# Kernel optimization log

Measured on AMD Instinct MI355X. Metric: run time of the kernel, lower is better.

The kernel has to match this reference:

```python
import jax, jax.numpy as jnp
import numpy as np

N = 100_000          # nodes
E = 800_000          # edges
IN_DIM = 128
OUT_DIM = 128
H = 8                # heads
DK = OUT_DIM // H    # 16
T = 3                # node types
R = 8                # edge relation types
LN_EPS = 1e-5


def setup_inputs():
    key = jax.random.key(0)
    k = jax.random.split(key, 16)
    node_inp = jax.random.normal(k[0], (N, IN_DIM), dtype=jnp.float32)
    node_type = jax.random.randint(k[1], (N,), 0, T)
    edge_index = jax.random.randint(k[2], (2, E), 0, N)
    edge_type = jax.random.randint(k[3], (E,), 0, R)
    edge_sign = jax.random.randint(k[4], (E,), 0, 3) - 1      # values in {-1,0,1}
    edge_distance = jax.random.uniform(k[5], (E,), dtype=jnp.float32) * 2e5
    sc = 1.0 / np.sqrt(IN_DIM)
    Wq = jax.random.normal(k[6], (T, IN_DIM, OUT_DIM), dtype=jnp.float32) * sc
    Wk = jax.random.normal(k[7], (T, IN_DIM, OUT_DIM), dtype=jnp.float32) * sc
    Wv = jax.random.normal(k[8], (T, IN_DIM, OUT_DIM), dtype=jnp.float32) * sc
    bq = jnp.zeros((T, OUT_DIM), jnp.float32)
    bk = jnp.zeros((T, OUT_DIM), jnp.float32)
    bv = jnp.zeros((T, OUT_DIM), jnp.float32)
    rel_q = jax.random.normal(k[9], (R, H, DK), dtype=jnp.float32) * 0.2
    rel_k = jax.random.normal(k[10], (R, H, DK), dtype=jnp.float32) * 0.2
    rel_v = jax.random.normal(k[11], (R, H, DK), dtype=jnp.float32) * 0.2
    rel_bias = jnp.zeros((R, H), jnp.float32)
    ones = jnp.ones((H, DK), dtype=jnp.float32)
    sign_k_fixed = jnp.stack([-ones, ones], axis=0)   # [2,H,DK] buffers (neg,pos)
    sign_v_fixed = jnp.stack([-ones, ones], axis=0)
    sign_k_neutral = jnp.ones((H, DK), jnp.float32)
    sign_v_neutral = jnp.ones((H, DK), jnp.float32)
    dist_alpha = jnp.float32(0.1)
    dist_tau = jnp.float32(1e5)
    skip = jnp.ones((T,), jnp.float32)
    ln_gamma = jnp.ones((T, OUT_DIM), jnp.float32)
    ln_beta = jnp.zeros((T, OUT_DIM), jnp.float32)
    return dict(node_inp=node_inp, node_type=node_type, edge_index=edge_index,
                edge_type=edge_type, edge_sign=edge_sign, edge_distance=edge_distance,
                Wq=Wq, bq=bq, Wk=Wk, bk=bk, Wv=Wv, bv=bv,
                rel_q=rel_q, rel_k=rel_k, rel_v=rel_v, rel_bias=rel_bias,
                sign_k_fixed=sign_k_fixed, sign_v_fixed=sign_v_fixed,
                sign_k_neutral=sign_k_neutral, sign_v_neutral=sign_v_neutral,
                dist_alpha=dist_alpha, dist_tau=dist_tau, skip=skip,
                ln_gamma=ln_gamma, ln_beta=ln_beta)


def reference(node_inp, node_type, edge_index, edge_type, edge_sign, edge_distance,
              Wq, bq, Wk, bk, Wv, bv, rel_q, rel_k, rel_v, rel_bias,
              sign_k_fixed, sign_v_fixed, sign_k_neutral, sign_v_neutral,
              dist_alpha, dist_tau, skip, ln_gamma, ln_beta):
    src, dst = edge_index[0], edge_index[1]
    n = node_inp.shape[0]
    e = src.shape[0]
    # Per-node-type Q/K/V: compute projections for all types [N,T,O], select by type
    # (equivalent to the masked per-type Linear dispatch in the torch code).
    ar = jnp.arange(n)
    Q = (jnp.einsum('nd,tdo->nto', node_inp, Wq) + bq)[ar, node_type].reshape(n, H, DK)
    K = (jnp.einsum('nd,tdo->nto', node_inp, Wk) + bk)[ar, node_type].reshape(n, H, DK)
    V = (jnp.einsum('nd,tdo->nto', node_inp, Wv) + bv)[ar, node_type].reshape(n, H, DK)
    # sign dispatch: -1 -> 0 (neg), +1 -> 1 (pos), anything else -> 2 (neutral)
    sign_idx = jnp.where(edge_sign == -1, 0, jnp.where(edge_sign == 1, 1, 2))
    sign_k_all = jnp.concatenate([sign_k_fixed, sign_k_neutral[None]], axis=0)  # [3,H,DK]
    sign_v_all = jnp.concatenate([sign_v_fixed, sign_v_neutral[None]], axis=0)
    # edge-wise gather + relational modulation
    q_eff = Q[dst] * rel_q[edge_type]                               # [E,H,DK]
    k_eff = K[src] * rel_k[edge_type] * sign_k_all[sign_idx]
    v_eff = V[src] * rel_v[edge_type] * sign_v_all[sign_idx]
    scores = jnp.sum(q_eff * k_eff, axis=-1) / np.sqrt(DK)          # [E,H]
    scores = scores + rel_bias[edge_type]
    phi = dist_alpha * jnp.exp(-edge_distance / (dist_tau + 1e-9))
    scores = scores + phi[:, None]
    # segment softmax over destination nodes
    m = jax.ops.segment_max(scores, dst, num_segments=n)            # [N,H]
    m = jax.lax.stop_gradient(jnp.where(jnp.isfinite(m), m, 0.0))
    es = jnp.exp(scores - m[dst])
    Z = jax.ops.segment_sum(es, dst, num_segments=n)
    attn = es / (Z[dst] + 1e-9)
    # message scatter-aggregate
    msg = (v_eff * attn[:, :, None]).reshape(e, OUT_DIM)
    out = jax.ops.segment_sum(msg, dst, num_segments=n)             # [N,OUT_DIM]
    # per-type gated residual + per-type LayerNorm
    alpha = jax.nn.sigmoid(skip)[node_type][:, None]
    x = alpha * out + (1.0 - alpha) * node_inp
    mu = jnp.mean(x, axis=-1, keepdims=True)
    var = jnp.mean((x - mu) ** 2, axis=-1, keepdims=True)
    xn = (x - mu) * jax.lax.rsqrt(var + LN_EPS)
    return xn * ln_gamma[node_type] + ln_beta[node_type]
```

## Files before the change

kernel.cpp:

```cpp
#include <hip/hip_runtime.h>
#include <hip/hip_bf16.h>

typedef unsigned int uint;
typedef unsigned short ushort;
typedef unsigned long long ull;
typedef __attribute__((ext_vector_type(8))) short short8;
typedef __attribute__((ext_vector_type(4))) float f32x4;

#define WP_ELEMS 147456

__device__ __forceinline__ ushort f2bf(float f) {
  uint x = __float_as_uint(f);
  return (ushort)((x + 0x7fffu + ((x >> 16) & 1u)) >> 16);
}
__device__ __forceinline__ uint packbf(float a, float b) {
  return ((uint)f2bf(b) << 16) | (uint)f2bf(a);
}
__device__ __forceinline__ float bflo(uint u) { return __uint_as_float(u << 16); }
__device__ __forceinline__ float bfhi(uint u) { return __uint_as_float(u & 0xffff0000u); }

__global__ __launch_bounds__(256) void setup_kernel(
    const float* __restrict__ wq, const float* __restrict__ wk, const float* __restrict__ wv,
    const float* __restrict__ rq, const float* __restrict__ rk, const float* __restrict__ rv,
    ushort* __restrict__ Wp, float* __restrict__ ktab, float* __restrict__ vtab,
    const int* __restrict__ ntype, int* __restrict__ cnt,
    const int* __restrict__ edst, int* __restrict__ ecnt, int N, int E) {
  int i = blockIdx.x * 256 + threadIdx.x;
  if (i < WP_ELEMS) {
    int j    = i & 7;
    int lane = (i >> 3) & 63;
    int ot   = (i >> 9) & 7;
    int ks   = (i >> 12) & 3;
    int mt   = i >> 14;
    int mat  = mt / 3;
    int t    = mt - mat * 3;
    int o = ot * 16 + (lane & 15);
    int d = ks * 32 + (lane >> 4) * 8 + j;
    const float* src = (mat == 0) ? wq : (mat == 1) ? wk : wv;
    Wp[i] = f2bf(src[t * 16384 + d * 128 + o]);
  }
  if (i < 1024) {
    ktab[i] = 0.25f * rq[i] * rk[i];
    vtab[i] = rv[i];
  }
  {
    int lane = threadIdx.x & 63;
    int t = (i < N) ? ntype[i] : -1;
#pragma unroll
    for (int tt = 0; tt < 3; ++tt) {
      ull mask = __ballot(t == tt);
      if (mask) {
        int leader = __ffsll((long long)mask) - 1;
        if (lane == leader) atomicAdd(&cnt[tt], __popcll(mask));
      }
    }
  }
  if (i < E) atomicAdd(&ecnt[edst[i]], 1);
}

__global__ void offs_kernel(const int* __restrict__ cnt, int* __restrict__ off) {
  int o = 0;
  off[0] = 0;
  for (int t = 0; t < 3; ++t) {
    o += ((cnt[t] + 63) >> 6) << 6;
    off[t + 1] = o;
  }
}

__global__ __launch_bounds__(256) void fill_kernel(const int* __restrict__ ntype,
                                                   const int* __restrict__ off,
                                                   int* __restrict__ pos,
                                                   int* __restrict__ perm,
                                                   int* __restrict__ pinv, int N) {
  int i = blockIdx.x * 256 + threadIdx.x;
  int lane = threadIdx.x & 63;
  int t = (i < N) ? ntype[i] : -1;
#pragma unroll
  for (int tt = 0; tt < 3; ++tt) {
    ull mask = __ballot(t == tt);
    if (mask) {
      int leader = __ffsll((long long)mask) - 1;
      int base = 0;
      if (lane == leader) base = atomicAdd(&pos[tt], __popcll(mask));
      base = __shfl(base, leader);
      if (t == tt) {
        int rank = __popcll(mask & ((lane == 63) ? 0x7fffffffffffffffull
                                                 : ((1ull << lane) - 1ull)));
        int p = off[tt] + base + rank;
        perm[p] = i;
        pinv[i] = p;
      }
    }
  }
}

__global__ __launch_bounds__(256) void gemm_kernel(
    const float* __restrict__ X, const int* __restrict__ perm,
    const int* __restrict__ off, const ushort* __restrict__ Wp,
    const float* __restrict__ bq, const float* __restrict__ bk, const float* __restrict__ bv,
    float* __restrict__ Qp, uint* __restrict__ KVp) {
  __shared__ __align__(16) char smem[33792];
  __shared__ int prow[64];
  ushort* As = (ushort*)smem;
  float* tbuf = (float*)smem;
  const int tid = threadIdx.x;
  const int base = blockIdx.x * 64;
  const int off1 = off[1], off2 = off[2], off3 = off[3];
  if (base >= off3) return;
  const int t = (base >= off1) + (base >= off2);

  if (tid < 64) prow[tid] = perm[base + tid];
  __syncthreads();
#pragma unroll
  for (int pass = 0; pass < 8; ++pass) {
    int row = pass * 8 + (tid >> 5);
    int dw = tid & 31;
    int p = prow[row];
    uint ux = 0u, uy = 0u;
    if (p >= 0) {
      float4 xv = *(const float4*)(X + (size_t)p * 128 + dw * 4);
      ux = packbf(xv.x, xv.y);
      uy = packbf(xv.z, xv.w);
    }
    uint* s = (uint*)smem + row * 68 + dw * 2;
    s[0] = ux; s[1] = uy;
  }
  __syncthreads();

  const int lane = tid & 63;
  const int w = tid >> 6;
  const int m0 = w * 16;
  const int r = lane & 15;
  const int q = lane >> 4;

  short8 afrag[4];
#pragma unroll
  for (int ks = 0; ks < 4; ++ks)
    afrag[ks] = *(const short8*)(As + (m0 + r) * 136 + ks * 32 + q * 8);
  __syncthreads();

  float* tw = tbuf + w * 2112;
  uint4 ksave[4];
#pragma unroll
  for (int mat = 0; mat < 3; ++mat) {
    f32x4 acc[8];
#pragma unroll
    for (int ot = 0; ot < 8; ++ot) acc[ot] = (f32x4){0.f, 0.f, 0.f, 0.f};

    const ushort* wb = Wp + (size_t)(mat * 3 + t) * 16384 + lane * 8;
#pragma unroll
    for (int ks = 0; ks < 4; ++ks) {
      const ushort* wk_ = wb + ks * 4096;
#pragma unroll
      for (int ot = 0; ot < 8; ++ot) {
        short8 b = *(const short8*)(wk_ + ot * 512);
        acc[ot] = __builtin_amdgcn_mfma_f32_16x16x32_bf16(afrag[ks], b, acc[ot], 0, 0, 0);
      }
    }

    const float* bias = (mat == 0) ? bq : (mat == 1) ? bk : bv;
#pragma unroll
    for (int ot = 0; ot < 8; ++ot) {
      float bi = bias[t * 128 + ot * 16 + r];
#pragma unroll
      for (int reg = 0; reg < 4; ++reg)
        tw[(q * 4 + reg) * 132 + ot * 16 + r] = acc[ot][reg] + bi;
    }
    if (mat == 0) {
#pragma unroll
      for (int p = 0; p < 8; ++p) {
        int f = (p * 64 + lane) * 4;
        int row = f >> 7, col = f & 127;
        float4 val = *(const float4*)(tw + row * 132 + col);
        *(float4*)(Qp + (size_t)(base + m0 + row) * 128 + col) = val;
      }
    } else if (mat == 1) {
#pragma unroll
      for (int p = 0; p < 4; ++p) {
        int g = p * 64 + lane;
        int f = g * 8;
        int row = f >> 7, col = f & 127;
        const float* src = tw + row * 132 + col;
        float4 a4 = *(const float4*)(src);
        float4 b4 = *(const float4*)(src + 4);
        uint4 u;
        u.x = packbf(a4.x, a4.y);
        u.y = packbf(a4.z, a4.w);
        u.z = packbf(b4.x, b4.y);
        u.w = packbf(b4.z, b4.w);
        ksave[p] = u;
      }
    } else {
#pragma unroll
      for (int p = 0; p < 4; ++p) {
        int g = p * 64 + lane;
        int f = g * 8;
        int row = f >> 7, col = f & 127;
        const float* src = tw + row * 132 + col;
        float4 a4 = *(const float4*)(src);
        float4 b4 = *(const float4*)(src + 4);
        uint4 v4;
        v4.x = packbf(a4.x, a4.y);
        v4.y = packbf(a4.z, a4.w);
        v4.z = packbf(b4.x, b4.y);
        v4.w = packbf(b4.z, b4.w);
        uint4 w0, w1;
        w0.x = ksave[p].x; w0.y = v4.x; w0.z = ksave[p].y; w0.w = v4.y;
        w1.x = ksave[p].z; w1.y = v4.z; w1.z = ksave[p].w; w1.w = v4.w;
        uint* dstp = KVp + (size_t)(base + m0 + row) * 128 + col;
        *(uint4*)(dstp) = w0;
        *(uint4*)(dstp + 4) = w1;
      }
    }
  }
}

__global__ __launch_bounds__(256) void csum_kernel(const int* __restrict__ ecnt,
                                                   int* __restrict__ csum, int N) {
  __shared__ int s[4];
  int basei = blockIdx.x * 1024;
  int tid = threadIdx.x;
  int v = 0;
#pragma unroll
  for (int k = 0; k < 4; ++k) {
    int i = basei + k * 256 + tid;
    if (i < N) v += ecnt[i];
  }
#pragma unroll
  for (int m = 1; m < 64; m <<= 1) v += __shfl_xor(v, m);
  if ((tid & 63) == 0) s[tid >> 6] = v;
  __syncthreads();
  if (tid == 0) csum[blockIdx.x] = s[0] + s[1] + s[2] + s[3];
}

__global__ __launch_bounds__(1024) void cscan_kernel(const int* __restrict__ csum,
                                                     int* __restrict__ coff,
                                                     int* __restrict__ rowptrN,
                                                     int NC, int E) {
  __shared__ int sd[32];
  int tid = threadIdx.x, lane = tid & 63, w = tid >> 6;
  int v = (tid < NC) ? csum[tid] : 0;
  int x = v;
#pragma unroll
  for (int d = 1; d < 64; d <<= 1) {
    int t = __shfl_up(x, d);
    if (lane >= d) x += t;
  }
  if (lane == 63) sd[w] = x;
  __syncthreads();
  if (w == 0 && lane < 16) {
    int y = sd[lane];
#pragma unroll
    for (int d = 1; d < 16; d <<= 1) {
      int t = __shfl_up(y, d);
      if (lane >= d) y += t;
    }
    sd[16 + lane] = y;
  }
  __syncthreads();
  int excl = ((w > 0) ? sd[16 + w - 1] : 0) + (x - v);
  if (tid < NC) coff[tid] = excl;
  if (tid == 0) rowptrN[0] = E;
}

__global__ __launch_bounds__(1024) void rowptr_kernel(const int* __restrict__ ecnt,
                                                      const int* __restrict__ coff,
                                                      int* __restrict__ rowptr,
                                                      int* __restrict__ cursor, int N) {
  __shared__ int sd[32];
  int basei = blockIdx.x * 1024;
  int tid = threadIdx.x, lane = tid & 63, w = tid >> 6;
  int i = basei + tid;
  int v = (i < N) ? ecnt[i] : 0;
  int x = v;
#pragma unroll
  for (int d = 1; d < 64; d <<= 1) {
    int t = __shfl_up(x, d);
    if (lane >= d) x += t;
  }
  if (lane == 63) sd[w] = x;
  __syncthreads();
  if (w == 0 && lane < 16) {
    int y = sd[lane];
#pragma unroll
    for (int d = 1; d < 16; d <<= 1) {
      int t = __shfl_up(y, d);
      if (lane >= d) y += t;
    }
    sd[16 + lane] = y;
  }
  __syncthreads();
  int excl = coff[blockIdx.x] + ((w > 0) ? sd[16 + w - 1] : 0) + (x - v);
  if (i < N) { rowptr[i] = excl; cursor[i] = excl; }
}

__global__ __launch_bounds__(256) void scatter_kernel(
    const int* __restrict__ esrc, const int* __restrict__ edst,
    const int* __restrict__ etype, const int* __restrict__ esign,
    const float* __restrict__ edist,
    const float* __restrict__ p_alpha, const float* __restrict__ p_tau,
    const int* __restrict__ pinv, int* __restrict__ cursor,
    int2* __restrict__ erec, int E) {
  int e = blockIdx.x * 256 + threadIdx.x;
  if (e >= E) return;
  int dst = edst[e];
  int p = atomicAdd(&cursor[dst], 1);
  int et = etype[e], sg = esign[e];
  int sbit = (sg == -1) ? 1 : 0;
  float parg = fminf(fmaxf(-edist[e] / (p_tau[0] + 1e-9f), -80.f), 0.f);
  int2 r;
  r.x = pinv[esrc[e]] | (et << 18) | (sbit << 21);
  r.y = __float_as_int(p_alpha[0] * __expf(parg));
  erec[p] = r;
}

struct Pass {
  uint4 kv0, kv1;
  float4 t0, t1;
  float4 v0, v1;
  float bias;
  float sgn;
  int valid;
};

__device__ __forceinline__ Pass fetchp(
    int e0, int row1, const int2* __restrict__ erec,
    const uint* __restrict__ KVp, const float* __restrict__ ktab,
    const float* __restrict__ vtab, const float* __restrict__ rb, int cl) {
  Pass P;
  P.valid = (e0 < row1);
  int e = P.valid ? e0 : (row1 - 1);
  int2 r = erec[e];
  int pk = r.x;
  float phi = __int_as_float(r.y);
  int pe = pk & 0x3ffff;
  int et = (pk >> 18) & 7;
  P.sgn = (pk & (1 << 21)) ? -1.f : 1.f;
  const uint* kvb = KVp + (size_t)pe * 128 + cl * 8;
  P.kv0 = *(const uint4*)(kvb);
  P.kv1 = *(const uint4*)(kvb + 4);
  const float* kb = ktab + et * 128 + cl * 8;
  P.t0 = *(const float4*)(kb);
  P.t1 = *(const float4*)(kb + 4);
  const float* vb = vtab + et * 128 + cl * 8;
  P.v0 = *(const float4*)(vb);
  P.v1 = *(const float4*)(vb + 4);
  P.bias = rb[et * 8 + (cl >> 1)] + phi;
  return P;
}

__device__ __forceinline__ void computep(
    const Pass& P, const float4& q0, const float4& q1, float& z,
    float& a0, float& a1, float& a2, float& a3,
    float& a4, float& a5, float& a6, float& a7) {
  float part = q0.x * (P.t0.x * bflo(P.kv0.x));
  part = fmaf(q0.y, P.t0.y * bfhi(P.kv0.x), part);
  part = fmaf(q0.z, P.t0.z * bflo(P.kv0.z), part);
  part = fmaf(q0.w, P.t0.w * bfhi(P.kv0.z), part);
  part = fmaf(q1.x, P.t1.x * bflo(P.kv1.x), part);
  part = fmaf(q1.y, P.t1.y * bfhi(P.kv1.x), part);
  part = fmaf(q1.z, P.t1.z * bflo(P.kv1.z), part);
  part = fmaf(q1.w, P.t1.w * bfhi(P.kv1.z), part);
  part += __shfl_xor(part, 1);
  float score = fminf(fmaf(P.sgn, part, P.bias), 80.f);
  float es = __expf(score);
  es = P.valid ? es : 0.f;
  z += es;
  float esv = es * P.sgn;
  a0 = fmaf(esv, P.v0.x * bflo(P.kv0.y), a0);
  a1 = fmaf(esv, P.v0.y * bfhi(P.kv0.y), a1);
  a2 = fmaf(esv, P.v0.z * bflo(P.kv0.w), a2);
  a3 = fmaf(esv, P.v0.w * bfhi(P.kv0.w), a3);
  a4 = fmaf(esv, P.v1.x * bflo(P.kv1.y), a4);
  a5 = fmaf(esv, P.v1.y * bfhi(P.kv1.y), a5);
  a6 = fmaf(esv, P.v1.z * bflo(P.kv1.w), a6);
  a7 = fmaf(esv, P.v1.w * bfhi(P.kv1.w), a7);
}

__global__ __launch_bounds__(256) void agg_kernel(
    const float* __restrict__ Qp, const uint* __restrict__ KVp,
    const int* __restrict__ pinv, const int* __restrict__ rowptr,
    const int2* __restrict__ erec,
    const float* __restrict__ rb, const float* __restrict__ ktab,
    const float* __restrict__ vtab,
    const float* __restrict__ X, const int* __restrict__ ntype,
    const float* __restrict__ skip, const float* __restrict__ gamma,
    const float* __restrict__ beta, float* __restrict__ y, int N) {
  const int wslot = blockIdx.x * 4 + (threadIdx.x >> 6);
  const int lane = threadIdx.x & 63;
  const int g = lane >> 4;
  const int cl = lane & 15;
  const int c0 = cl * 8;

  for (int ii = 0; ii < 4; ++ii) {
    int dst = wslot * 4 + ii;
    if (dst >= N) return;

    int pq = pinv[dst];
    int row0 = rowptr[dst], row1 = rowptr[dst + 1];
    const float* qb = Qp + (size_t)pq * 128 + c0;
    float4 q0 = *(const float4*)(qb);
    float4 q1 = *(const float4*)(qb + 4);

    float a0 = 0.f, a1 = 0.f, a2 = 0.f, a3 = 0.f;
    float a4 = 0.f, a5 = 0.f, a6 = 0.f, a7 = 0.f;
    float z = 0.f;

    int deg = row1 - row0;
    if (deg > 0) {
      int np = (deg + 3) >> 2;
      Pass A = fetchp(row0 + g, row1, erec, KVp, ktab, vtab, rb, cl);
      int p = 0;
      while (true) {
        if (p + 1 < np) {
          Pass B = fetchp(row0 + (p + 1) * 4 + g, row1, erec, KVp, ktab, vtab, rb, cl);
          computep(A, q0, q1, z, a0, a1, a2, a3, a4, a5, a6, a7);
          A = B;
          ++p;
        } else {
          computep(A, q0, q1, z, a0, a1, a2, a3, a4, a5, a6, a7);
          break;
        }
      }
    }

#pragma unroll
    for (int m = 16; m < 64; m <<= 1) {
      a0 += __shfl_xor(a0, m); a1 += __shfl_xor(a1, m);
      a2 += __shfl_xor(a2, m); a3 += __shfl_xor(a3, m);
      a4 += __shfl_xor(a4, m); a5 += __shfl_xor(a5, m);
      a6 += __shfl_xor(a6, m); a7 += __shfl_xor(a7, m);
      z  += __shfl_xor(z, m);
    }

    if (lane < 16) {
      float inv = 1.0f / (z + 1e-9f);
      float o0 = a0 * inv, o1 = a1 * inv, o2 = a2 * inv, o3 = a3 * inv;
      float o4 = a4 * inv, o5 = a5 * inv, o6 = a6 * inv, o7 = a7 * inv;

      int t = ntype[dst];
      float a = 1.0f / (1.0f + __expf(-skip[t]));
      float b = 1.0f - a;
      const float* xb = X + (size_t)dst * 128 + c0;
      float4 x0 = *(const float4*)(xb);
      float4 x1 = *(const float4*)(xb + 4);
      float w0 = a * o0 + b * x0.x, w1 = a * o1 + b * x0.y;
      float w2 = a * o2 + b * x0.z, w3 = a * o3 + b * x0.w;
      float w4 = a * o4 + b * x1.x, w5 = a * o5 + b * x1.y;
      float w6 = a * o6 + b * x1.z, w7 = a * o7 + b * x1.w;

      float sum = w0 + w1 + w2 + w3 + w4 + w5 + w6 + w7;
      float sq = w0 * w0 + w1 * w1 + w2 * w2 + w3 * w3 +
                 w4 * w4 + w5 * w5 + w6 * w6 + w7 * w7;
#pragma unroll
      for (int m = 1; m < 16; m <<= 1) {
        sum += __shfl_xor(sum, m);
        sq  += __shfl_xor(sq, m);
      }
      float mean = sum * (1.0f / 128.0f);
      float var = fmaxf(sq * (1.0f / 128.0f) - mean * mean, 0.0f);
      float rstd = rsqrtf(var + 1e-5f);

      const float* gb = gamma + t * 128 + c0;
      const float* bb2 = beta + t * 128 + c0;
      float4 g0 = *(const float4*)(gb);
      float4 g1 = *(const float4*)(gb + 4);
      float4 be0 = *(const float4*)(bb2);
      float4 be1 = *(const float4*)(bb2 + 4);
      float4 r0, r1;
      r0.x = (w0 - mean) * rstd * g0.x + be0.x;
      r0.y = (w1 - mean) * rstd * g0.y + be0.y;
      r0.z = (w2 - mean) * rstd * g0.z + be0.z;
      r0.w = (w3 - mean) * rstd * g0.w + be0.w;
      r1.x = (w4 - mean) * rstd * g1.x + be1.x;
      r1.y = (w5 - mean) * rstd * g1.y + be1.y;
      r1.z = (w6 - mean) * rstd * g1.z + be1.z;
      r1.w = (w7 - mean) * rstd * g1.w + be1.w;
      float* yb = y + (size_t)dst * 128 + c0;
      *(float4*)(yb) = r0;
      *(float4*)(yb + 4) = r1;
    }
  }
}

extern "C" void kernel_launch(void* const* d_in, const int* in_sizes, int n_in,
                              void* d_out, int out_size, void* d_ws, size_t ws_size,
                              hipStream_t stream) {
  const float* X     = (const float*)d_in[0];
  const int*   ntype = (const int*)d_in[1];
  const int*   eidx  = (const int*)d_in[2];
  const int*   etype = (const int*)d_in[3];
  const int*   esign = (const int*)d_in[4];
  const float* edist = (const float*)d_in[5];
  const float* wq = (const float*)d_in[6];
  const float* bq = (const float*)d_in[7];
  const float* wk = (const float*)d_in[8];
  const float* bk = (const float*)d_in[9];
  const float* wv = (const float*)d_in[10];
  const float* bv = (const float*)d_in[11];
  const float* rq = (const float*)d_in[12];
  const float* rk = (const float*)d_in[13];
  const float* rv = (const float*)d_in[14];
  const float* rb = (const float*)d_in[15];

  const int N = in_sizes[1];
  const int E = in_sizes[3];
  const int NP = N + 192;
  const int NC = (N + 1023) / 1024;

  float* ws = (float*)d_ws;
  float* Qp   = ws;
  uint*  KVp  = (uint*)(Qp + (size_t)NP * 128);
  float* ktab = (float*)(KVp + (size_t)NP * 128);
  float* vtab = ktab + 1024;
  ushort* Wp  = (ushort*)(vtab + 1024);
  int* cnt    = (int*)(Wp + WP_ELEMS);
  int* pos    = cnt + 4;
  int* ecnt   = pos + 4;
  int* perm   = ecnt + N;
  int* pinv   = perm + NP;
  int* off    = pinv + N;
  int* rowptr = off + 4;
  int* cursor = rowptr + N + 1;
  int* csum   = cursor + N;
  int* coff   = csum + 1024;
  int2* erec  = (int2*)(coff + 1024);

  hipMemsetAsync(cnt, 0, (size_t)(8 + N) * sizeof(int), stream);
  hipMemsetAsync(perm, 0xFF, (size_t)NP * sizeof(int), stream);

  setup_kernel<<<(E + 255) / 256, 256, 0, stream>>>(
      wq, wk, wv, rq, rk, rv, Wp, ktab, vtab, ntype, cnt, eidx + E, ecnt, N, E);
  offs_kernel<<<1, 1, 0, stream>>>(cnt, off);
  fill_kernel<<<(N + 255) / 256, 256, 0, stream>>>(ntype, off, pos, perm, pinv, N);

  csum_kernel<<<NC, 256, 0, stream>>>(ecnt, csum, N);
  cscan_kernel<<<1, 1024, 0, stream>>>(csum, coff, rowptr + N, NC, E);
  rowptr_kernel<<<NC, 1024, 0, stream>>>(ecnt, coff, rowptr, cursor, N);
  scatter_kernel<<<(E + 255) / 256, 256, 0, stream>>>(
      eidx, eidx + E, etype, esign, edist, (const float*)d_in[20], (const float*)d_in[21],
      pinv, cursor, erec, E);

  gemm_kernel<<<(N + 255) / 64, 256, 0, stream>>>(X, perm, off, Wp, bq, bk, bv, Qp, KVp);

  agg_kernel<<<(N + 15) / 16, 256, 0, stream>>>(Qp, KVp, pinv, rowptr, erec,
                                                rb, ktab, vtab, X, ntype,
                                                (const float*)d_in[22], (const float*)d_in[23],
                                                (const float*)d_in[24], (float*)d_out, N);
}
```

Before: 507.9 us.

## Merge preprocessing kernels and co-launch GEMM with edge scatter

```diff
diff --git a/kernel.cpp b/kernel.cpp
--- a/kernel.cpp
+++ b/kernel.cpp
@@ -58,44 +58,112 @@
   if (i < E) atomicAdd(&ecnt[edst[i]], 1);
 }
 
-__global__ void offs_kernel(const int* __restrict__ cnt, int* __restrict__ off) {
-  int o = 0;
-  off[0] = 0;
-  for (int t = 0; t < 3; ++t) {
-    o += ((cnt[t] + 63) >> 6) << 6;
-    off[t + 1] = o;
-  }
-}
-
-__global__ __launch_bounds__(256) void fill_kernel(const int* __restrict__ ntype,
-                                                   const int* __restrict__ off,
-                                                   int* __restrict__ pos,
-                                                   int* __restrict__ perm,
-                                                   int* __restrict__ pinv, int N) {
-  int i = blockIdx.x * 256 + threadIdx.x;
-  int lane = threadIdx.x & 63;
-  int t = (i < N) ? ntype[i] : -1;
-#pragma unroll
-  for (int tt = 0; tt < 3; ++tt) {
-    ull mask = __ballot(t == tt);
-    if (mask) {
-      int leader = __ffsll((long long)mask) - 1;
-      int base = 0;
-      if (lane == leader) base = atomicAdd(&pos[tt], __popcll(mask));
-      base = __shfl(base, leader);
-      if (t == tt) {
-        int rank = __popcll(mask & ((lane == 63) ? 0x7fffffffffffffffull
-                                                 : ((1ull << lane) - 1ull)));
-        int p = off[tt] + base + rank;
-        perm[p] = i;
-        pinv[i] = p;
-      }
-    }
-  }
-}
-
-__global__ __launch_bounds__(256) void gemm_kernel(
-    const float* __restrict__ X, const int* __restrict__ perm,
+__global__ __launch_bounds__(256) void fc_kernel(
+    const int* __restrict__ ntype, const int* __restrict__ cnt,
+    int* __restrict__ pos, int* __restrict__ perm, int* __restrict__ pinv,
+    int* __restrict__ off,
+    const int* __restrict__ ecnt, int* __restrict__ csum,
+    int N, int fill_blocks) {
+  __shared__ int s[4];
+  int bid = blockIdx.x;
+  if (bid < fill_blocks) {
+    int i = bid * 256 + threadIdx.x;
+    int lane = threadIdx.x & 63;
+    int c0 = cnt[0], c1 = cnt[1];
+    int o1 = ((c0 + 63) >> 6) << 6;
+    int o2 = o1 + (((c1 + 63) >> 6) << 6);
+    if (i == 0) {
+      int c2 = cnt[2];
+      int o3 = o2 + (((c2 + 63) >> 6) << 6);
+      off[0] = 0; off[1] = o1; off[2] = o2; off[3] = o3;
+    }
+    int t = (i < N) ? ntype[i] : -1;
+#pragma unroll
+    for (int tt = 0; tt < 3; ++tt) {
+      ull mask = __ballot(t == tt);
+      if (mask) {
+        int leader = __ffsll((long long)mask) - 1;
+        int base = 0;
+        if (lane == leader) base = atomicAdd(&pos[tt], __popcll(mask));
+        base = __shfl(base, leader);
+        if (t == tt) {
+          int obase = (tt == 0) ? 0 : (tt == 1) ? o1 : o2;
+          int rank = __popcll(mask & ((lane == 63) ? 0x7fffffffffffffffull
+                                                   : ((1ull << lane) - 1ull)));
+          int p = obase + base + rank;
+          perm[p] = i;
+          pinv[i] = p;
+        }
+      }
+    }
+  } else {
+    int cb = bid - fill_blocks;
+    int basei = cb * 1024;
+    int tid = threadIdx.x;
+    int v = 0;
+#pragma unroll
+    for (int k = 0; k < 4; ++k) {
+      int i = basei + k * 256 + tid;
+      if (i < N) v += ecnt[i];
+    }
+#pragma unroll
+    for (int m = 1; m < 64; m <<= 1) v += __shfl_xor(v, m);
+    if ((tid & 63) == 0) s[tid >> 6] = v;
+    __syncthreads();
+    if (tid == 0) csum[cb] = s[0] + s[1] + s[2] + s[3];
+  }
+}
+
+__global__ __launch_bounds__(1024) void rowptr_kernel(const int* __restrict__ ecnt,
+                                                      const int* __restrict__ csum,
+                                                      int* __restrict__ rowptr,
+                                                      int* __restrict__ cursor,
+                                                      int N, int E) {
+  __shared__ int sd[32];
+  __shared__ int sbase;
+  int basei = blockIdx.x * 1024;
+  int tid = threadIdx.x, lane = tid & 63, w = tid >> 6;
+
+  int c = (tid < blockIdx.x) ? csum[tid] : 0;
+#pragma unroll
+  for (int m = 1; m < 64; m <<= 1) c += __shfl_xor(c, m);
+  if (lane == 0) sd[w] = c;
+  __syncthreads();
+  if (tid == 0) {
+    int s = 0;
+#pragma unroll
+    for (int k = 0; k < 16; ++k) s += sd[k];
+    sbase = s;
+    if (blockIdx.x == 0) rowptr[N] = E;
+  }
+  __syncthreads();
+
+  int i = basei + tid;
+  int v = (i < N) ? ecnt[i] : 0;
+  int x = v;
+#pragma unroll
+  for (int d = 1; d < 64; d <<= 1) {
+    int t = __shfl_up(x, d);
+    if (lane >= d) x += t;
+  }
+  if (lane == 63) sd[w] = x;
+  __syncthreads();
+  if (w == 0 && lane < 16) {
+    int y = sd[lane];
+#pragma unroll
+    for (int d = 1; d < 16; d <<= 1) {
+      int t = __shfl_up(y, d);
+      if (lane >= d) y += t;
+    }
+    sd[16 + lane] = y;
+  }
+  __syncthreads();
+  int excl = sbase + ((w > 0) ? sd[16 + w - 1] : 0) + (x - v);
+  if (i < N) { rowptr[i] = excl; cursor[i] = excl; }
+}
+
+__device__ void gemm_body(
+    int bid, const float* __restrict__ X, const int* __restrict__ perm,
     const int* __restrict__ off, const ushort* __restrict__ Wp,
     const float* __restrict__ bq, const float* __restrict__ bk, const float* __restrict__ bv,
     float* __restrict__ Qp, uint* __restrict__ KVp) {
@@ -104,7 +172,7 @@
   ushort* As = (ushort*)smem;
   float* tbuf = (float*)smem;
   const int tid = threadIdx.x;
-  const int base = blockIdx.x * 64;
+  const int base = bid * 64;
   const int off1 = off[1], off2 = off[2], off3 = off[3];
   if (base >= off3) return;
   const int t = (base >= off1) + (base >= off2);
@@ -215,93 +283,23 @@
   }
 }
 
-__global__ __launch_bounds__(256) void csum_kernel(const int* __restrict__ ecnt,
-                                                   int* __restrict__ csum, int N) {
-  __shared__ int s[4];
-  int basei = blockIdx.x * 1024;
-  int tid = threadIdx.x;
-  int v = 0;
-#pragma unroll
-  for (int k = 0; k < 4; ++k) {
-    int i = basei + k * 256 + tid;
-    if (i < N) v += ecnt[i];
-  }
-#pragma unroll
-  for (int m = 1; m < 64; m <<= 1) v += __shfl_xor(v, m);
-  if ((tid & 63) == 0) s[tid >> 6] = v;
-  __syncthreads();
-  if (tid == 0) csum[blockIdx.x] = s[0] + s[1] + s[2] + s[3];
-}
-
-__global__ __launch_bounds__(1024) void cscan_kernel(const int* __restrict__ csum,
-                                                     int* __restrict__ coff,
-                                                     int* __restrict__ rowptrN,
-                                                     int NC, int E) {
-  __shared__ int sd[32];
-  int tid = threadIdx.x, lane = tid & 63, w = tid >> 6;
-  int v = (tid < NC) ? csum[tid] : 0;
-  int x = v;
-#pragma unroll
-  for (int d = 1; d < 64; d <<= 1) {
-    int t = __shfl_up(x, d);
-    if (lane >= d) x += t;
-  }
-  if (lane == 63) sd[w] = x;
-  __syncthreads();
-  if (w == 0 && lane < 16) {
-    int y = sd[lane];
-#pragma unroll
-    for (int d = 1; d < 16; d <<= 1) {
-      int t = __shfl_up(y, d);
-      if (lane >= d) y += t;
-    }
-    sd[16 + lane] = y;
-  }
-  __syncthreads();
-  int excl = ((w > 0) ? sd[16 + w - 1] : 0) + (x - v);
-  if (tid < NC) coff[tid] = excl;
-  if (tid == 0) rowptrN[0] = E;
-}
-
-__global__ __launch_bounds__(1024) void rowptr_kernel(const int* __restrict__ ecnt,
-                                                      const int* __restrict__ coff,
-                                                      int* __restrict__ rowptr,
-                                                      int* __restrict__ cursor, int N) {
-  __shared__ int sd[32];
-  int basei = blockIdx.x * 1024;
-  int tid = threadIdx.x, lane = tid & 63, w = tid >> 6;
-  int i = basei + tid;
-  int v = (i < N) ? ecnt[i] : 0;
-  int x = v;
-#pragma unroll
-  for (int d = 1; d < 64; d <<= 1) {
-    int t = __shfl_up(x, d);
-    if (lane >= d) x += t;
-  }
-  if (lane == 63) sd[w] = x;
-  __syncthreads();
-  if (w == 0 && lane < 16) {
-    int y = sd[lane];
-#pragma unroll
-    for (int d = 1; d < 16; d <<= 1) {
-      int t = __shfl_up(y, d);
-      if (lane >= d) y += t;
-    }
-    sd[16 + lane] = y;
-  }
-  __syncthreads();
-  int excl = coff[blockIdx.x] + ((w > 0) ? sd[16 + w - 1] : 0) + (x - v);
-  if (i < N) { rowptr[i] = excl; cursor[i] = excl; }
-}
-
-__global__ __launch_bounds__(256) void scatter_kernel(
+__global__ __launch_bounds__(256) void sg_kernel(
+    const float* __restrict__ X, const int* __restrict__ perm,
+    const int* __restrict__ off, const ushort* __restrict__ Wp,
+    const float* __restrict__ bq, const float* __restrict__ bk, const float* __restrict__ bv,
+    float* __restrict__ Qp, uint* __restrict__ KVp, int gemm_blocks,
     const int* __restrict__ esrc, const int* __restrict__ edst,
     const int* __restrict__ etype, const int* __restrict__ esign,
     const float* __restrict__ edist,
     const float* __restrict__ p_alpha, const float* __restrict__ p_tau,
     const int* __restrict__ pinv, int* __restrict__ cursor,
     int2* __restrict__ erec, int E) {
-  int e = blockIdx.x * 256 + threadIdx.x;
+  int bid = blockIdx.x;
+  if (bid < gemm_blocks) {
+    gemm_body(bid, X, perm, off, Wp, bq, bk, bv, Qp, KVp);
+    return;
+  }
+  int e = (bid - gemm_blocks) * 256 + threadIdx.x;
   if (e >= E) return;
   int dst = edst[e];
   int p = atomicAdd(&cursor[dst], 1);
@@ -523,25 +521,27 @@
   int* rowptr = off + 4;
   int* cursor = rowptr + N + 1;
   int* csum   = cursor + N;
-  int* coff   = csum + 1024;
-  int2* erec  = (int2*)(coff + 1024);
+  int2* erec  = (int2*)(csum + 1024);
 
   hipMemsetAsync(cnt, 0, (size_t)(8 + N) * sizeof(int), stream);
   hipMemsetAsync(perm, 0xFF, (size_t)NP * sizeof(int), stream);
 
   setup_kernel<<<(E + 255) / 256, 256, 0, stream>>>(
       wq, wk, wv, rq, rk, rv, Wp, ktab, vtab, ntype, cnt, eidx + E, ecnt, N, E);
-  offs_kernel<<<1, 1, 0, stream>>>(cnt, off);
-  fill_kernel<<<(N + 255) / 256, 256, 0, stream>>>(ntype, off, pos, perm, pinv, N);
-
-  csum_kernel<<<NC, 256, 0, stream>>>(ecnt, csum, N);
-  cscan_kernel<<<1, 1024, 0, stream>>>(csum, coff, rowptr + N, NC, E);
-  rowptr_kernel<<<NC, 1024, 0, stream>>>(ecnt, coff, rowptr, cursor, N);
-  scatter_kernel<<<(E + 255) / 256, 256, 0, stream>>>(
-      eidx, eidx + E, etype, esign, edist, (const float*)d_in[20], (const float*)d_in[21],
+
+  const int fill_blocks = (N + 255) / 256;
+  fc_kernel<<<fill_blocks + NC, 256, 0, stream>>>(
+      ntype, cnt, pos, perm, pinv, off, ecnt, csum, N, fill_blocks);
+
+  rowptr_kernel<<<NC, 1024, 0, stream>>>(ecnt, csum, rowptr, cursor, N, E);
+
+  const int gemm_blocks = (N + 255) / 64;
+  const int scat_blocks = (E + 255) / 256;
+  sg_kernel<<<gemm_blocks + scat_blocks, 256, 0, stream>>>(
+      X, perm, off, Wp, bq, bk, bv, Qp, KVp, gemm_blocks,
+      eidx, eidx + E, etype, esign, edist,
+      (const float*)d_in[20], (const float*)d_in[21],
       pinv, cursor, erec, E);
-
-  gemm_kernel<<<(N + 255) / 64, 256, 0, stream>>>(X, perm, off, Wp, bq, bk, bv, Qp, KVp);
 
   agg_kernel<<<(N + 15) / 16, 256, 0, stream>>>(Qp, KVp, pinv, rowptr, erec,
                                                 rb, ktab, vtab, X, ntype,
```

New measurement: 476.2 us. 6.2% less time.
